# Performance work log

Measured on AMD Instinct MI355X. Metric: run time of the kernel, lower is better.

Reference implementation:

```python
import jax, jax.numpy as jnp
import numpy as np

B, T, C, H = 4096, 128, 128, 64  # T must equal BLOCK_SIZE=128, C=EMBEDDING_DIM=128


def setup_inputs() -> dict:
    key = jax.random.key(0)
    k1, k2, k3, k4, k5, k6 = jax.random.split(key, 6)
    source_embedding = jax.random.normal(k1, (B, T, C), dtype=jnp.float32)
    target_embedding = jax.random.normal(k2, (B, T, C), dtype=jnp.float32)
    # realistic padding: positions < length are valid; guarantees col 0 valid (no NaN rows)
    lengths = jax.random.randint(k3, (B,), 1, T + 1)
    pad_mask = jnp.arange(T)[None, :] < lengths[:, None]  # (B, T) bool
    Wq = jax.random.normal(k4, (C, H), dtype=jnp.float32) * 0.02
    Wk = jax.random.normal(k5, (C, H), dtype=jnp.float32) * 0.02
    Wv = jax.random.normal(k6, (C, H), dtype=jnp.float32) * 0.02
    return {"source_embedding": source_embedding, "target_embedding": target_embedding,
            "pad_mask": pad_mask, "Wq": Wq, "Wk": Wk, "Wv": Wv}


def reference(source_embedding, target_embedding, pad_mask, Wq, Wk, Wv):
    # q from target, k/v from source (cross-attention capable), bias-free projections
    q = target_embedding @ Wq   # (B, T, H)
    k = source_embedding @ Wk   # (B, T, H)
    v = source_embedding @ Wv   # (B, T, H)
    scale = k.shape[-1] ** -0.5
    wei = jnp.einsum('btd,bsd->bts', q, k) * scale  # (B, T, T)
    causal = jnp.tril(jnp.ones((T, T), dtype=bool))  # needs_future_mask=True
    mask = pad_mask[:, None, :] & causal[None, :, :]  # fuse pad + future masks
    wei = jnp.where(mask, wei, -jnp.inf)
    wei = jax.nn.softmax(wei, axis=-1)
    # dropout disabled (eval mode) for deterministic reference
    out = wei @ v  # (B, T, H)
    return out
```

## Files before the change

### kernel.cpp

```cpp
#include <hip/hip_runtime.h>
#include <stdint.h>


typedef uint32_t u32x2 __attribute__((ext_vector_type(2)));
typedef uint32_t u32x4 __attribute__((ext_vector_type(4)));
typedef float    f32x4 __attribute__((ext_vector_type(4)));
typedef __bf16   bf16x8 __attribute__((ext_vector_type(8)));

static __device__ __forceinline__ uint32_t pack2(float a, float b) {
  uint32_t ua = __builtin_bit_cast(uint32_t, a);
  uint32_t ub = __builtin_bit_cast(uint32_t, b);
  ua += 0x7FFFu + ((ua >> 16) & 1u);
  ub += 0x7FFFu + ((ub >> 16) & 1u);
  return (ua >> 16) | (ub & 0xFFFF0000u);
}
static __device__ __forceinline__ uint32_t cvt2(float a, float b) {
  uint16_t lo = __builtin_bit_cast(uint16_t, (__bf16)a);
  uint16_t hi = __builtin_bit_cast(uint16_t, (__bf16)b);
  return (uint32_t)lo | ((uint32_t)hi << 16);
}
static __device__ __forceinline__ f32x4 mfma16(u32x4 a, u32x4 b, f32x4 c) {
  return __builtin_amdgcn_mfma_f32_16x16x32_bf16(
      __builtin_bit_cast(bf16x8, a), __builtin_bit_cast(bf16x8, b), c, 0, 0, 0);
}

__global__ void prep_w(const float* __restrict__ Wq, const float* __restrict__ Wk,
                       const float* __restrict__ Wv, const void* __restrict__ mask,
                       uint32_t* __restrict__ ws) {
  const int blk = blockIdx.x;
  const int l = threadIdx.x;
  if (blk < 48) {
    const int m  = blk >> 4;
    const int ct = (blk >> 2) & 3;
    const int ks = blk & 3;
    const float* W = (m == 0) ? Wq : ((m == 1) ? Wk : Wv);
    const int h  = ct * 16 + (l & 15);
    const int c0 = ks * 32 + (l >> 4) * 8;
    u32x4 v;
#pragma unroll
    for (int p = 0; p < 4; ++p)
      v[p] = pack2(W[(c0 + 2 * p) * 64 + h], W[(c0 + 2 * p + 1) * 64 + h]);
    ((u32x4*)ws)[blk * 64 + l] = v;
  } else {
    const uint32_t* mw = (const uint32_t*)mask;
    int fl = 0;
    for (int i = l * 16; i < l * 16 + 16; ++i) {
      uint32_t x = mw[i];
      if (x == 0x3F800000u) fl = 2;
      else if (x > 1u && fl != 2) fl = 1;
    }
#pragma unroll
    for (int off = 32; off > 0; off >>= 1) {
      int o = __shfl_down(fl, off);
      fl = (o > fl) ? o : fl;
    }
    if (l == 0) ws[12288] = (uint32_t)fl;
  }
}

__global__ __launch_bounds__(512, 4) void attn_fused(
    const float* __restrict__ src, const float* __restrict__ tgt,
    const void* __restrict__ mask, const uint32_t* __restrict__ ws,
    float* __restrict__ out) {
  __shared__ __align__(16) uint8_t lds[66048];
  uint8_t* const EMB = lds;
  uint8_t* const Qb  = lds + 16384;
  uint8_t* const Kb  = lds + 32768;
  uint8_t* const Vb  = lds + 49152;
  float*  const BIAS = (float*)(lds + 65536);

  const int b   = blockIdx.x;
  const int tid = (int)threadIdx.x;
  const int l   = tid & 63;
  const int w   = tid >> 6;
  const int l15 = l & 15;
  const int g4  = l >> 4;
  const int ct  = w & 3;
  const int sg  = (w >> 2) * 2;

  const u32x4* wsv = (const u32x4*)ws;
  const int mflag = (int)ws[12288];
  const float* const srcb = src + (size_t)b * 16384;
  const float* const tgtb = tgt + (size_t)b * 16384;

  u32x4 wk[4], wv[4], wq[4];
#pragma unroll
  for (int ks = 0; ks < 4; ++ks) {
    wk[ks] = wsv[((4 + ct) * 4 + ks) * 64 + l];
    wv[ks] = wsv[((8 + ct) * 4 + ks) * 64 + l];
  }

  f32x4 pf[4];
  auto stage_load = [&](const float* gbase) {
#pragma unroll
    for (int p = 0; p < 4; ++p)
      pf[p] = *(const f32x4*)(gbase + tid * 4 + p * 2048);
  };
  auto stage_write = [&]() {
#pragma unroll
    for (int p = 0; p < 4; ++p) {
      const int c   = tid + p * 512;
      const int row = c >> 5;
      const int cc  = c & 31;
      u32x2 d = { cvt2(pf[p][0], pf[p][1]), cvt2(pf[p][2], pf[p][3]) };
      *(u32x2*)(EMB + (row << 8) + ((((cc >> 1) ^ (row & 7))) << 4) + ((cc & 1) << 3)) = d;
    }
  };

  auto projKV = [&](int half) {
#pragma unroll
    for (int i = 0; i < 2; ++i) {
      const int st  = sg + i;
      const int row = st * 16 + l15;
      f32x4 cK = {0, 0, 0, 0}, cV = {0, 0, 0, 0};
#pragma unroll
      for (int ks = 0; ks < 4; ++ks) {
        u32x4 e = *(const u32x4*)(EMB + (row << 8) + ((((ks * 4 + g4) ^ (row & 7))) << 4));
        cK = mfma16(wk[ks], e, cK);
        cV = mfma16(e, wv[ks], cV);
      }
      const int s  = half * 64 + st * 16 + l15;
      const int h0 = ct * 16 + g4 * 4;
      u32x2 dk = { cvt2(cK[0], cK[1]), cvt2(cK[2], cK[3]) };
      *(u32x2*)(Kb + (s << 7) + ((((h0 >> 3) ^ (s & 7))) << 4) + ((h0 & 7) << 1)) = dk;
      const int s0 = half * 64 + st * 16 + g4 * 4;
      const int h  = ct * 16 + l15;
      u32x2 dv = { cvt2(cV[0], cV[1]), cvt2(cV[2], cV[3]) };
      *(u32x2*)(Vb + (h << 8) + ((((s0 >> 3) ^ (h & 7))) << 4) + ((s0 & 7) << 1)) = dv;
    }
  };
  auto projQ = [&](int half) {
#pragma unroll
    for (int i = 0; i < 2; ++i) {
      const int st  = sg + i;
      const int row = st * 16 + l15;
      f32x4 cQ = {0, 0, 0, 0};
#pragma unroll
      for (int ks = 0; ks < 4; ++ks) {
        u32x4 e = *(const u32x4*)(EMB + (row << 8) + ((((ks * 4 + g4) ^ (row & 7))) << 4));
        cQ = mfma16(wq[ks], e, cQ);
      }
      const int t  = half * 64 + st * 16 + l15;
      const int h0 = ct * 16 + g4 * 4;
      u32x2 dq = { cvt2(cQ[0], cQ[1]), cvt2(cQ[2], cQ[3]) };
      *(u32x2*)(Qb + (t << 7) + ((((h0 >> 3) ^ (t & 7))) << 4) + ((h0 & 7) << 1)) = dq;
    }
  };

  stage_load(srcb);
  float biasv = 0.0f;
  if (tid < 128) {
    bool valid;
    if (mflag == 1)      valid = ((const uint8_t*)mask)[b * 128 + tid] != 0;
    else if (mflag == 0) valid = ((const int*)mask)[b * 128 + tid] != 0;
    else                 valid = ((const float*)mask)[b * 128 + tid] != 0.0f;
    biasv = valid ? 0.0f : -1e30f;
  }
  stage_write();
  if (tid < 128) BIAS[tid] = biasv;
  __syncthreads();
  stage_load(srcb + 8192);
  projKV(0);
  __syncthreads();
  stage_write();
  __syncthreads();
  stage_load(tgtb);
  projKV(1);
#pragma unroll
  for (int ks = 0; ks < 4; ++ks)
    wq[ks] = wsv[(ct * 4 + ks) * 64 + l];
  __syncthreads();
  stage_write();
  __syncthreads();
  stage_load(tgtb + 8192);
  projQ(0);
  __syncthreads();
  stage_write();
  __syncthreads();
  projQ(1);
  __syncthreads();

  const int tq = 16 * w + l15;
  u32x4 qf0 = *(const u32x4*)(Qb + (tq << 7) + (((g4 ^ (tq & 7))) << 4));
  u32x4 qf1 = *(const u32x4*)(Qb + (tq << 7) + ((((4 + g4) ^ (tq & 7))) << 4));

  f32x4 sacc[8];
#pragma unroll
  for (int mt = 0; mt < 8; ++mt) sacc[mt] = {0, 0, 0, 0};
  __builtin_amdgcn_s_setprio(1);
#pragma unroll
  for (int mt = 0; mt < 8; ++mt) {
    const int srow = mt * 16 + l15;
    u32x4 k0 = *(const u32x4*)(Kb + (srow << 7) + (((g4 ^ (srow & 7))) << 4));
    u32x4 k1 = *(const u32x4*)(Kb + (srow << 7) + ((((4 + g4) ^ (srow & 7))) << 4));
    sacc[mt] = mfma16(k0, qf0, sacc[mt]);
    sacc[mt] = mfma16(k1, qf1, sacc[mt]);
  }
  __builtin_amdgcn_s_setprio(0);

  float m = -3.0e38f;
#pragma unroll
  for (int mt = 0; mt < 8; ++mt) {
    f32x4 b4 = *(const f32x4*)(BIAS + mt * 16 + g4 * 4);
#pragma unroll
    for (int r = 0; r < 4; ++r) {
      float v = sacc[mt][r] * 0.125f + b4[r];
      sacc[mt][r] = v;
      m = fmaxf(m, v);
    }
  }
  m = fmaxf(m, __shfl_xor(m, 16));
  m = fmaxf(m, __shfl_xor(m, 32));
  float sum = 0.0f;
#pragma unroll
  for (int mt = 0; mt < 8; ++mt) {
#pragma unroll
    for (int r = 0; r < 4; ++r) {
      const int s = mt * 16 + g4 * 4 + r;
      float p = __expf(sacc[mt][r] - m);
      p = (s <= tq) ? p : 0.0f;
      sacc[mt][r] = p;
      sum += p;
    }
  }
  sum += __shfl_xor(sum, 16);
  sum += __shfl_xor(sum, 32);
  const float inv = 1.0f / sum;

  uint8_t* const Pr = (l15 < 8) ? (EMB + w * 2048 + l15 * 256)
                                : (Qb + w * 2048 + (l15 - 8) * 256);
#pragma unroll
  for (int mt = 0; mt < 8; ++mt) {
    u32x2 d = { cvt2(sacc[mt][0], sacc[mt][1]), cvt2(sacc[mt][2], sacc[mt][3]) };
    const int c = mt * 2 + (g4 >> 1);
    *(u32x2*)(Pr + (((c ^ l15)) << 4) + ((g4 & 1) << 3)) = d;
  }

  f32x4 oacc[4];
#pragma unroll
  for (int vt = 0; vt < 4; ++vt) oacc[vt] = {0, 0, 0, 0};
  __builtin_amdgcn_s_setprio(1);
#pragma unroll
  for (int ks = 0; ks < 4; ++ks) {
    u32x4 pb = *(const u32x4*)(Pr + ((((ks * 4 + g4) ^ l15)) << 4));
#pragma unroll
    for (int vt = 0; vt < 4; ++vt) {
      const int vrow = vt * 16 + l15;
      u32x4 vf = *(const u32x4*)(Vb + (vrow << 8) + ((((ks * 4 + g4) ^ (vrow & 7))) << 4));
      oacc[vt] = mfma16(vf, pb, oacc[vt]);
    }
  }
  __builtin_amdgcn_s_setprio(0);

  float* const ob = out + (size_t)b * 8192 + (size_t)tq * 64;
#pragma unroll
  for (int vt = 0; vt < 4; ++vt) {
    f32x4 o = { oacc[vt][0] * inv, oacc[vt][1] * inv,
                oacc[vt][2] * inv, oacc[vt][3] * inv };
    *(f32x4*)(ob + vt * 16 + g4 * 4) = o;
  }
}

extern "C" void kernel_launch(void* const* d_in, const int* in_sizes, int n_in,
                              void* d_out, int out_size, void* d_ws, size_t ws_size,
                              hipStream_t stream) {
  const float* src = (const float*)d_in[0];
  const float* tgt = (const float*)d_in[1];
  const void*  msk = d_in[2];
  const float* Wq  = (const float*)d_in[3];
  const float* Wk  = (const float*)d_in[4];
  const float* Wv  = (const float*)d_in[5];
  uint32_t* ws = (uint32_t*)d_ws;
  float* out = (float*)d_out;
  const int B = in_sizes[0] / (128 * 128);

  hipLaunchKernelGGL(prep_w, dim3(49), dim3(64), 0, stream, Wq, Wk, Wv, msk, ws);
  hipLaunchKernelGGL(attn_fused, dim3(B), dim3(512), 0, stream,
                     src, tgt, msk, ws, out);
}
```

Baseline: 142.1 us.

## Double-buffer embedding staging in LDS and load mask bias into registers

Splits the single embedding staging buffer into two LDS buffers and keeps two register sets of prefetched global data. This halves the number of block barriers in the projection phase and lets loads run further ahead of compute. The pad-mask bias is now read straight from global memory into per-lane registers instead of going through an LDS bias array. In exchange, LDS grows to 80KB and the launch bound drops to 2 blocks per CU, which lowers occupancy and adds register pressure.

```diff
diff --git a/kernel.cpp b/kernel.cpp
--- a/kernel.cpp
+++ b/kernel.cpp
@@ -58,16 +58,16 @@
   }
 }
 
-__global__ __launch_bounds__(512, 4) void attn_fused(
+__global__ __launch_bounds__(512, 2) void attn_fused(
     const float* __restrict__ src, const float* __restrict__ tgt,
     const void* __restrict__ mask, const uint32_t* __restrict__ ws,
     float* __restrict__ out) {
-  __shared__ __align__(16) uint8_t lds[66048];
-  uint8_t* const EMB = lds;
-  uint8_t* const Qb  = lds + 16384;
-  uint8_t* const Kb  = lds + 32768;
-  uint8_t* const Vb  = lds + 49152;
-  float*  const BIAS = (float*)(lds + 65536);
+  __shared__ __align__(16) uint8_t lds[81920];
+  uint8_t* const X0 = lds;
+  uint8_t* const X1 = lds + 16384;
+  uint8_t* const Kb = lds + 32768;
+  uint8_t* const Vb = lds + 49152;
+  uint8_t* const Qb = lds + 65536;
 
   const int b   = blockIdx.x;
   const int tid = (int)threadIdx.x;
@@ -90,24 +90,24 @@
     wv[ks] = wsv[((8 + ct) * 4 + ks) * 64 + l];
   }
 
-  f32x4 pf[4];
-  auto stage_load = [&](const float* gbase) {
+  f32x4 pfA[4], pfB[4];
+  auto stage_load = [&](const float* gbase, f32x4* pf) {
 #pragma unroll
     for (int p = 0; p < 4; ++p)
       pf[p] = *(const f32x4*)(gbase + tid * 4 + p * 2048);
   };
-  auto stage_write = [&]() {
+  auto stage_write = [&](uint8_t* X, const f32x4* pf) {
 #pragma unroll
     for (int p = 0; p < 4; ++p) {
       const int c   = tid + p * 512;
       const int row = c >> 5;
       const int cc  = c & 31;
       u32x2 d = { cvt2(pf[p][0], pf[p][1]), cvt2(pf[p][2], pf[p][3]) };
-      *(u32x2*)(EMB + (row << 8) + ((((cc >> 1) ^ (row & 7))) << 4) + ((cc & 1) << 3)) = d;
-    }
-  };
-
-  auto projKV = [&](int half) {
+      *(u32x2*)(X + (row << 8) + ((((cc >> 1) ^ (row & 7))) << 4) + ((cc & 1) << 3)) = d;
+    }
+  };
+
+  auto projKV = [&](const uint8_t* E, int half) {
 #pragma unroll
     for (int i = 0; i < 2; ++i) {
       const int st  = sg + i;
@@ -115,7 +115,7 @@
       f32x4 cK = {0, 0, 0, 0}, cV = {0, 0, 0, 0};
 #pragma unroll
       for (int ks = 0; ks < 4; ++ks) {
-        u32x4 e = *(const u32x4*)(EMB + (row << 8) + ((((ks * 4 + g4) ^ (row & 7))) << 4));
+        u32x4 e = *(const u32x4*)(E + (row << 8) + ((((ks * 4 + g4) ^ (row & 7))) << 4));
         cK = mfma16(wk[ks], e, cK);
         cV = mfma16(e, wv[ks], cV);
       }
@@ -129,7 +129,7 @@
       *(u32x2*)(Vb + (h << 8) + ((((s0 >> 3) ^ (h & 7))) << 4) + ((s0 & 7) << 1)) = dv;
     }
   };
-  auto projQ = [&](int half) {
+  auto projQ = [&](const uint8_t* E, int half) {
 #pragma unroll
     for (int i = 0; i < 2; ++i) {
       const int st  = sg + i;
@@ -137,7 +137,7 @@
       f32x4 cQ = {0, 0, 0, 0};
 #pragma unroll
       for (int ks = 0; ks < 4; ++ks) {
-        u32x4 e = *(const u32x4*)(EMB + (row << 8) + ((((ks * 4 + g4) ^ (row & 7))) << 4));
+        u32x4 e = *(const u32x4*)(E + (row << 8) + ((((ks * 4 + g4) ^ (row & 7))) << 4));
         cQ = mfma16(wq[ks], e, cQ);
       }
       const int t  = half * 64 + st * 16 + l15;
@@ -147,38 +147,45 @@
     }
   };
 
-  stage_load(srcb);
-  float biasv = 0.0f;
-  if (tid < 128) {
-    bool valid;
-    if (mflag == 1)      valid = ((const uint8_t*)mask)[b * 128 + tid] != 0;
-    else if (mflag == 0) valid = ((const int*)mask)[b * 128 + tid] != 0;
-    else                 valid = ((const float*)mask)[b * 128 + tid] != 0.0f;
-    biasv = valid ? 0.0f : -1e30f;
-  }
-  stage_write();
-  if (tid < 128) BIAS[tid] = biasv;
-  __syncthreads();
-  stage_load(srcb + 8192);
-  projKV(0);
-  __syncthreads();
-  stage_write();
-  __syncthreads();
-  stage_load(tgtb);
-  projKV(1);
+  stage_load(srcb, pfA);
+  stage_load(srcb + 8192, pfB);
+  stage_write(X0, pfA);
+  __syncthreads();
+  stage_load(tgtb, pfA);
+  projKV(X0, 0);
+  stage_write(X1, pfB);
+  __syncthreads();
+  stage_load(tgtb + 8192, pfB);
+  projKV(X1, 1);
 #pragma unroll
   for (int ks = 0; ks < 4; ++ks)
     wq[ks] = wsv[(ct * 4 + ks) * 64 + l];
-  __syncthreads();
-  stage_write();
-  __syncthreads();
-  stage_load(tgtb + 8192);
-  projQ(0);
-  __syncthreads();
-  stage_write();
-  __syncthreads();
-  projQ(1);
-  __syncthreads();
+  stage_write(X0, pfA);
+  __syncthreads();
+  projQ(X0, 0);
+  stage_write(X1, pfB);
+  __syncthreads();
+  projQ(X1, 1);
+  __syncthreads();
+
+  f32x4 bias[8];
+#pragma unroll
+  for (int mt = 0; mt < 8; ++mt) {
+    const int s0 = mt * 16 + g4 * 4;
+    if (mflag == 0) {
+      u32x4 mi = *(const u32x4*)((const int*)mask + (size_t)b * 128 + s0);
+#pragma unroll
+      for (int r = 0; r < 4; ++r) bias[mt][r] = mi[r] ? 0.0f : -1e30f;
+    } else if (mflag == 1) {
+      uint32_t mi = *(const uint32_t*)((const uint8_t*)mask + (size_t)b * 128 + s0);
+#pragma unroll
+      for (int r = 0; r < 4; ++r) bias[mt][r] = ((mi >> (8 * r)) & 0xFFu) ? 0.0f : -1e30f;
+    } else {
+      f32x4 mv = *(const f32x4*)((const float*)mask + (size_t)b * 128 + s0);
+#pragma unroll
+      for (int r = 0; r < 4; ++r) bias[mt][r] = (mv[r] != 0.0f) ? 0.0f : -1e30f;
+    }
+  }
 
   const int tq = 16 * w + l15;
   u32x4 qf0 = *(const u32x4*)(Qb + (tq << 7) + (((g4 ^ (tq & 7))) << 4));
@@ -201,10 +208,9 @@
   float m = -3.0e38f;
 #pragma unroll
   for (int mt = 0; mt < 8; ++mt) {
-    f32x4 b4 = *(const f32x4*)(BIAS + mt * 16 + g4 * 4);
 #pragma unroll
     for (int r = 0; r < 4; ++r) {
-      float v = sacc[mt][r] * 0.125f + b4[r];
+      float v = sacc[mt][r] * 0.125f + bias[mt][r];
       sacc[mt][r] = v;
       m = fmaxf(m, v);
     }
@@ -227,8 +233,8 @@
   sum += __shfl_xor(sum, 32);
   const float inv = 1.0f / sum;
 
-  uint8_t* const Pr = (l15 < 8) ? (EMB + w * 2048 + l15 * 256)
-                                : (Qb + w * 2048 + (l15 - 8) * 256);
+  uint8_t* const Pr = (l15 < 8) ? (X0 + w * 2048 + l15 * 256)
+                                : (X1 + w * 2048 + (l15 - 8) * 256);
 #pragma unroll
   for (int mt = 0; mt < 8; ++mt) {
     u32x2 d = { cvt2(sacc[mt][0], sacc[mt][1]), cvt2(sacc[mt][2], sacc[mt][3]) };
```

Measured after the change: 161.2 us. +13.5%, slower.
